# Performance work log

Measured on AMD Instinct MI355X. Metric: run time of the kernel, lower is better.

The kernel has to match this reference:

```python
import jax, jax.numpy as jnp
import numpy as np

N = 50000          # number of rows / ego agents
A = 65             # num_agents + 1 (slot dimension)
DEG = 32           # neighbors per row
EMB = 32           # embedding_dim
HID = 16           # mlp hidden (mlp_pre_pool_dims = [32, 16, 32])
BOT = 32           # bottleneck_dim = h_dim
NEG_INF = -jnp.inf


def setup_inputs() -> dict:
    key = jax.random.key(0)
    ks = jax.random.split(key, 8)
    corr_index = jax.random.normal(ks[0], (N, A, 2), dtype=jnp.float32)
    lstm_state = jax.random.normal(ks[1], (N, BOT), dtype=jnp.float32)
    # edge list with unique (row, slot) pairs so scatter-set is well defined
    col0 = np.repeat(np.arange(N, dtype=np.int32), DEG)
    col2 = np.tile(np.arange(DEG, dtype=np.int32), N)
    col1 = np.random.default_rng(1).integers(0, A, size=N * DEG).astype(np.int32)
    nei_index = jnp.asarray(np.stack([col0, col1, col2], axis=1))  # [E,3]
    # parameters (Linear weights stored as [in, out])
    def lin(k, fin, fout):
        bound = 1.0 / np.sqrt(fin)
        kw, kb = jax.random.split(k)
        W = jax.random.uniform(kw, (fin, fout), jnp.float32, -bound, bound)
        b = jax.random.uniform(kb, (fout,), jnp.float32, -bound, bound)
        return W, b
    W_se, b_se = lin(ks[2], 2, EMB)
    W1, b1 = lin(ks[3], EMB, HID)
    W2, b2 = lin(ks[4], HID, BOT)
    return {"corr_index": corr_index, "nei_index": nei_index,
            "lstm_state": lstm_state, "W_se": W_se, "b_se": b_se,
            "W1": W1, "b1": b1, "W2": W2, "b2": b2}


def reference(corr_index, nei_index, lstm_state, W_se, b_se, W1, b1, W2, b2):
    # gather relative positions for each edge: [E, 2]
    rel = corr_index[nei_index[:, 0], nei_index[:, 1]]
    # spatial embedding + MLP (Linear+ReLU, Linear+ReLU)
    r_t = rel @ W_se + b_se                         # [E, EMB]
    h = jax.nn.relu(r_t @ W1 + b1)                  # [E, HID]
    h = jax.nn.relu(h @ W2 + b2)                    # [E, BOT]
    # scatter into dense -inf buffer, max over slot dim, zero out empty rows
    H = jnp.full((N, A, BOT), NEG_INF, dtype=h.dtype)
    H = H.at[nei_index[:, 0], nei_index[:, 2]].set(h, unique_indices=True)
    pool_h = jnp.max(H, axis=1)                     # [N, BOT]
    pool_h = jnp.where(jnp.isneginf(pool_h), 0.0, pool_h)
    return pool_h
```

## Files before the change

### kernel.cpp

```cpp
#include <hip/hip_runtime.h>

#define NODES 50000
#define NA    65
#define NDEG  32


typedef float v2f __attribute__((ext_vector_type(2)));

static __device__ __forceinline__ v2f pk_fma(v2f a, v2f b, v2f c) {
    return __builtin_elementwise_fma(a, b, c);
}
static __device__ __forceinline__ v2f pk_max(v2f a, v2f b) {
    return __builtin_elementwise_max(a, b);
}

#define RELSTRIDE 34

__global__ __launch_bounds__(256, 1) void fused_kernel(
    const float* __restrict__ corr,
    const int*   __restrict__ nei,
    const float* __restrict__ W_se,
    const float* __restrict__ b_se,
    const float* __restrict__ W1,
    const float* __restrict__ b1,
    const float* __restrict__ W2,
    const float* __restrict__ b2,
    float* __restrict__ out)
{
    __shared__ __align__(16) float  fold[48];
    __shared__ __align__(16) float2 relbuf[32 * RELSTRIDE];

    int t  = threadIdx.x;
    int nb = blockIdx.x * 32;

    if (t < 48) {
        float s;
        if (t < 32) {
            int c = t >> 4, j = t & 15;
            s = 0.0f;
#pragma unroll
            for (int e = 0; e < 32; ++e)
                s = fmaf(W_se[c * 32 + e], W1[e * 16 + j], s);
        } else {
            int j = t - 32;
            s = b1[j];
#pragma unroll
            for (int e = 0; e < 32; ++e)
                s = fmaf(b_se[e], W1[e * 16 + j], s);
        }
        fold[t] = s;
    }

#pragma unroll
    for (int u = 0; u < 4; ++u) {
        int g    = t + 256 * u;
        int nl   = g >> 5;
        int d    = g & 31;
        int node = nb + nl;
        if (node < NODES) {
            int idx = nei[((size_t)node * NDEG + d) * 3 + 1];
            relbuf[nl * RELSTRIDE + d] =
                ((const float2*)corr)[(size_t)node * NA + idx];
        }
    }
    __syncthreads();

    int nl   = t >> 3;
    int node = nb + nl;
    int k0   = (t & 7) * 4;
    if (node >= NODES) return;

    v2f wc0v[8], wc1v[8], bcv[8];
    {
        const v2f* fv = (const v2f*)fold;
#pragma unroll
        for (int j = 0; j < 8; ++j) {
            wc0v[j] = fv[j];
            wc1v[j] = fv[8 + j];
            bcv[j]  = fv[16 + j];
        }
    }

#define W2T(p)                                                              \
    float4 ra_##p = *(const float4*)(W2 + (2 * (p)) * 32 + k0);             \
    float4 rb_##p = *(const float4*)(W2 + (2 * (p) + 1) * 32 + k0);         \
    v2f w2_##p##_0 = {ra_##p.x, rb_##p.x};                                  \
    v2f w2_##p##_1 = {ra_##p.y, rb_##p.y};                                  \
    v2f w2_##p##_2 = {ra_##p.z, rb_##p.z};                                  \
    v2f w2_##p##_3 = {ra_##p.w, rb_##p.w};
    W2T(0) W2T(1) W2T(2) W2T(3) W2T(4) W2T(5) W2T(6) W2T(7)
#undef W2T

    float4 b2v = *(const float4*)(b2 + k0);

    float vm0 = 0.0f, vm1 = 0.0f, vm2 = 0.0f, vm3 = 0.0f;

    const float2* rp = relbuf + nl * RELSTRIDE;

#define L2P(p) do {                                                         \
        acc0 = pk_fma(h1v[p], w2_##p##_0, acc0);                            \
        acc1 = pk_fma(h1v[p], w2_##p##_1, acc1);                            \
        acc2 = pk_fma(h1v[p], w2_##p##_2, acc2);                            \
        acc3 = pk_fma(h1v[p], w2_##p##_3, acc3);                            \
    } while (0)

#pragma unroll
    for (int d = 0; d < NDEG; ++d) {
        float2 r = rp[d];
        v2f r0s = {r.x, r.x}, r1s = {r.y, r.y};
        v2f h1v[8];
#pragma unroll
        for (int j = 0; j < 8; ++j)
            h1v[j] = pk_max((v2f)(0.0f),
                     pk_fma(r0s, wc0v[j], pk_fma(r1s, wc1v[j], bcv[j])));
        v2f acc0 = {b2v.x, 0.0f}, acc1 = {b2v.y, 0.0f};
        v2f acc2 = {b2v.z, 0.0f}, acc3 = {b2v.w, 0.0f};
        L2P(0); L2P(1); L2P(2); L2P(3); L2P(4); L2P(5); L2P(6); L2P(7);
        vm0 = fmaxf(vm0, acc0.x + acc0.y);
        vm1 = fmaxf(vm1, acc1.x + acc1.y);
        vm2 = fmaxf(vm2, acc2.x + acc2.y);
        vm3 = fmaxf(vm3, acc3.x + acc3.y);
    }
#undef L2P

    *(float4*)(out + (size_t)node * 32 + k0) = make_float4(vm0, vm1, vm2, vm3);
}

extern "C" void kernel_launch(void* const* d_in, const int* in_sizes, int n_in,
                              void* d_out, int out_size, void* d_ws, size_t ws_size,
                              hipStream_t stream) {
    const float* corr = (const float*)d_in[0];
    const int*   nei  = (const int*)d_in[1];
    const float* W_se = (const float*)d_in[3];
    const float* b_se = (const float*)d_in[4];
    const float* W1   = (const float*)d_in[5];
    const float* b1   = (const float*)d_in[6];
    const float* W2   = (const float*)d_in[7];
    const float* b2   = (const float*)d_in[8];
    float* out = (float*)d_out;

    int blocks = (NODES + 31) / 32;
    hipLaunchKernelGGL(fused_kernel, dim3(blocks), dim3(256), 0, stream,
                       corr, nei, W_se, b_se, W1, b1, W2, b2, out);
}
```

Measured before the change: 127.8 us.

## Compute second MLP layer with bf16 MFMA per node

Result: faster. 105.0 us (-17.8%).

```diff
diff --git a/kernel.cpp b/kernel.cpp
--- a/kernel.cpp
+++ b/kernel.cpp
@@ -1,4 +1,5 @@
 #include <hip/hip_runtime.h>
+#include <hip/hip_bf16.h>
 
 #define NODES 50000
 #define NA    65
@@ -6,6 +7,8 @@
 
 
 typedef float v2f __attribute__((ext_vector_type(2)));
+typedef __attribute__((ext_vector_type(8))) short short8;
+typedef __attribute__((ext_vector_type(16))) float f32x16;
 
 static __device__ __forceinline__ v2f pk_fma(v2f a, v2f b, v2f c) {
     return __builtin_elementwise_fma(a, b, c);
@@ -13,8 +16,6 @@
 static __device__ __forceinline__ v2f pk_max(v2f a, v2f b) {
     return __builtin_elementwise_max(a, b);
 }
-
-#define RELSTRIDE 34
 
 __global__ __launch_bounds__(256, 1) void fused_kernel(
     const float* __restrict__ corr,
@@ -28,7 +29,7 @@
     float* __restrict__ out)
 {
     __shared__ __align__(16) float  fold[48];
-    __shared__ __align__(16) float2 relbuf[32 * RELSTRIDE];
+    __shared__ __align__(16) float2 relbuf[32 * 32];
 
     int t  = threadIdx.x;
     int nb = blockIdx.x * 32;
@@ -59,71 +60,69 @@
         int node = nb + nl;
         if (node < NODES) {
             int idx = nei[((size_t)node * NDEG + d) * 3 + 1];
-            relbuf[nl * RELSTRIDE + d] =
-                ((const float2*)corr)[(size_t)node * NA + idx];
+            relbuf[nl * 32 + d] = ((const float2*)corr)[(size_t)node * NA + idx];
         }
     }
     __syncthreads();
 
-    int nl   = t >> 3;
-    int node = nb + nl;
-    int k0   = (t & 7) * 4;
-    if (node >= NODES) return;
+    int lane  = t & 63;
+    int w     = t >> 6;
+    int col   = lane & 31;
+    int khalf = lane >> 5;
 
-    v2f wc0v[8], wc1v[8], bcv[8];
+    v2f wc0v[4], wc1v[4], bcv[4];
     {
-        const v2f* fv = (const v2f*)fold;
+        const float* fb = fold + khalf * 8;
 #pragma unroll
-        for (int j = 0; j < 8; ++j) {
-            wc0v[j] = fv[j];
-            wc1v[j] = fv[8 + j];
-            bcv[j]  = fv[16 + j];
+        for (int p = 0; p < 4; ++p) {
+            wc0v[p] = *(const v2f*)(fb + 2 * p);
+            wc1v[p] = *(const v2f*)(fb + 16 + 2 * p);
+            bcv[p]  = *(const v2f*)(fb + 32 + 2 * p);
         }
     }
 
-#define W2T(p)                                                              \
-    float4 ra_##p = *(const float4*)(W2 + (2 * (p)) * 32 + k0);             \
-    float4 rb_##p = *(const float4*)(W2 + (2 * (p) + 1) * 32 + k0);         \
-    v2f w2_##p##_0 = {ra_##p.x, rb_##p.x};                                  \
-    v2f w2_##p##_1 = {ra_##p.y, rb_##p.y};                                  \
-    v2f w2_##p##_2 = {ra_##p.z, rb_##p.z};                                  \
-    v2f w2_##p##_3 = {ra_##p.w, rb_##p.w};
-    W2T(0) W2T(1) W2T(2) W2T(3) W2T(4) W2T(5) W2T(6) W2T(7)
-#undef W2T
+    union FragU { short8 s8; __hip_bfloat162 h2[4]; };
+    FragU bu;
+#pragma unroll
+    for (int p = 0; p < 4; ++p) {
+        int k = khalf * 8 + 2 * p;
+        bu.h2[p] = __float22bfloat162_rn(
+            make_float2(W2[k * 32 + col], W2[(k + 1) * 32 + col]));
+    }
+    float b2c = b2[col];
 
-    float4 b2v = *(const float4*)(b2 + k0);
+    f32x16 czero;
+#pragma unroll
+    for (int j = 0; j < 16; ++j) czero[j] = 0.0f;
 
-    float vm0 = 0.0f, vm1 = 0.0f, vm2 = 0.0f, vm3 = 0.0f;
-
-    const float2* rp = relbuf + nl * RELSTRIDE;
-
-#define L2P(p) do {                                                         \
-        acc0 = pk_fma(h1v[p], w2_##p##_0, acc0);                            \
-        acc1 = pk_fma(h1v[p], w2_##p##_1, acc1);                            \
-        acc2 = pk_fma(h1v[p], w2_##p##_2, acc2);                            \
-        acc3 = pk_fma(h1v[p], w2_##p##_3, acc3);                            \
-    } while (0)
+    const float2* rp = relbuf + w * 8 * 32;
 
 #pragma unroll
-    for (int d = 0; d < NDEG; ++d) {
-        float2 r = rp[d];
+    for (int i = 0; i < 8; ++i) {
+        int node = nb + w * 8 + i;
+        if (node >= NODES) break;
+
+        float2 r = rp[i * 32 + col];
         v2f r0s = {r.x, r.x}, r1s = {r.y, r.y};
-        v2f h1v[8];
+
+        FragU au;
 #pragma unroll
-        for (int j = 0; j < 8; ++j)
-            h1v[j] = pk_max((v2f)(0.0f),
-                     pk_fma(r0s, wc0v[j], pk_fma(r1s, wc1v[j], bcv[j])));
-        v2f acc0 = {b2v.x, 0.0f}, acc1 = {b2v.y, 0.0f};
-        v2f acc2 = {b2v.z, 0.0f}, acc3 = {b2v.w, 0.0f};
-        L2P(0); L2P(1); L2P(2); L2P(3); L2P(4); L2P(5); L2P(6); L2P(7);
-        vm0 = fmaxf(vm0, acc0.x + acc0.y);
-        vm1 = fmaxf(vm1, acc1.x + acc1.y);
-        vm2 = fmaxf(vm2, acc2.x + acc2.y);
-        vm3 = fmaxf(vm3, acc3.x + acc3.y);
+        for (int p = 0; p < 4; ++p) {
+            v2f h = pk_max((v2f)(0.0f),
+                     pk_fma(r0s, wc0v[p], pk_fma(r1s, wc1v[p], bcv[p])));
+            au.h2[p] = __float22bfloat162_rn(make_float2(h.x, h.y));
+        }
+
+        f32x16 acc = __builtin_amdgcn_mfma_f32_32x32x16_bf16(au.s8, bu.s8, czero, 0, 0, 0);
+
+        float m = acc[0];
+#pragma unroll
+        for (int j = 1; j < 16; ++j) m = fmaxf(m, acc[j]);
+        m = fmaxf(m, __shfl_xor(m, 32, 64));
+
+        float res = fmaxf(0.0f, m + b2c);
+        if (lane < 32) out[(size_t)node * 32 + col] = res;
     }
-#undef L2P
-
-    *(float4*)(out + (size_t)node * 32 + k0) = make_float4(vm0, vm1, vm2, vm3);
 }
 
 extern "C" void kernel_launch(void* const* d_in, const int* in_sizes, int n_in,
```
